# Kernel tuning notes

Measured on AMD Instinct MI355X. Metric: run time of the kernel, lower is better.

The kernel has to match this reference:

```python
import jax, jax.numpy as jnp
import numpy as np

# Balanced binary-tree tensorized circuit (CP sum-product layers), cirkit-style.
B, D, C, K, NCLS = 256, 256, 1, 256, 10
LEVELS = 8  # log2(D); each level halves the number of regions


def setup_inputs() -> dict:
    key = jax.random.key(0)
    ks = jax.random.split(key, LEVELS + 3)
    inp = {"x": jax.random.normal(ks[0], (B, D, C), dtype=jnp.float32)}
    # Input layer params: per-variable linear map C -> K units
    inp["W_in"] = jax.random.normal(ks[1], (D, C, K), dtype=jnp.float32)
    # CP layer params per tree level: (n_regions, arity=2, K_in, K_out)
    n = D
    for l in range(LEVELS):
        n //= 2
        inp[f"W_lvl{l}"] = jax.random.normal(ks[2 + l], (n, 2, K, K), dtype=jnp.float32)
    # Output mixing layer K -> num_classes
    inp["W_out"] = jax.random.normal(ks[2 + LEVELS], (K, NCLS), dtype=jnp.float32)
    return inp


def _circuit(x, W_in, W_lvls, W_out):
    # Input layers: gather scope (here: each var is its own scope) + per-var map.
    # (B, D, C) x (D, C, K) -> (B, D, K); tanh keeps units bounded in [-1, 1].
    h = jnp.tanh(jnp.einsum('bdc,dck->bdk', x, W_in))
    # Fused sum-product (CP) layers, one batched einsum per tree level instead of
    # a Python loop over individual small layers.
    for W in W_lvls:
        n = W.shape[0]
        hp = h.reshape(h.shape[0], n, 2, K)          # pair adjacent regions
        Wn = jax.nn.softmax(W, axis=2)               # reparam: convex sum over K_in
        proj = jnp.einsum('bnak,nakj->bnaj', hp, Wn) # per-child sum layer
        h = proj[:, :, 0, :] * proj[:, :, 1, :]      # Hadamard product layer
    root = h[:, 0, :]                                # (B, K)
    out = jnp.einsum('bk,kc->bc', root, jax.nn.softmax(W_out, axis=0))
    return out[:, None, :]                           # (B, num_out=1, num_cls)


def reference(x, W_in, W_lvl0, W_lvl1, W_lvl2, W_lvl3, W_lvl4, W_lvl5, W_lvl6, W_lvl7, W_out):
    W_lvls = [W_lvl0, W_lvl1, W_lvl2, W_lvl3, W_lvl4, W_lvl5, W_lvl6, W_lvl7]
    return _circuit(x, W_in, W_lvls, W_out)
```

## Files before the change

kernel.cpp:

```cpp
#include <hip/hip_runtime.h>

#define Bb 256
#define Kk 256
#define NCLS 10

typedef __attribute__((ext_vector_type(8))) short short8;
typedef __attribute__((ext_vector_type(4))) float f32x4;

__device__ __forceinline__ float bf2f(ushort u) {
    return __uint_as_float(((unsigned int)u) << 16);
}
__device__ __forceinline__ ushort f2bf(float f) {
    unsigned int u = __float_as_uint(f);
    u = (u + 0x7FFFu + ((u >> 16) & 1u)) >> 16;
    return (ushort)u;
}
__device__ __forceinline__ float tanh_fast(float v) {
    float t = __expf(2.f * v);
    return (t - 1.f) / (t + 1.f);
}

template<bool FIRST>
__global__ __launch_bounds__(256, 2)
void level_kernel(const float*  __restrict__ x,
                  const float*  __restrict__ Win,
                  const ushort* __restrict__ proj_prev,
                  const float*  __restrict__ W,
                  ushort*       __restrict__ proj_out,
                  int n)
{
    __shared__ __align__(16) ushort sA[256 * 40];
    __shared__ __align__(16) ushort sE[128 * 40];
    __shared__ float sRed[2][128];
    __shared__ float sRcp[128];

    const int tid = threadIdx.x;
    const int a   = blockIdx.x >> 1;
    const int jt  = blockIdx.x & 1;
    const int i   = blockIdx.y;
    const int d   = 2 * i + a;

    const int l   = tid & 63;
    const int l15 = l & 15;
    const int g   = l >> 4;
    const int w   = tid >> 6;
    const int wm  = w >> 1;
    const int wn  = w & 1;

    const int ej  = tid & 127;
    const int ekq = tid >> 7;

    f32x4 acc[8][4];
    #pragma unroll
    for (int mf = 0; mf < 8; ++mf)
        #pragma unroll
        for (int nf = 0; nf < 4; ++nf)
            acc[mf][nf] = (f32x4){0.f, 0.f, 0.f, 0.f};

    float csum = 0.f;

    const size_t wbase = ((size_t)(i * 2 + a)) * (size_t)(Kk * Kk);

    for (int k0 = 0; k0 < Kk; k0 += 32) {
        #pragma unroll
        for (int p = 0; p < 4; ++p) {
            const int unit = p * 256 + tid;
            const int m = unit >> 2;
            const int s = unit & 3;
            ushort pk[8];
            if (FIRST) {
                const float4 w0 = *(const float4*)&Win[(size_t)d * Kk + k0 + s * 8];
                const float4 w1 = *(const float4*)&Win[(size_t)d * Kk + k0 + s * 8 + 4];
                const float xv = x[(size_t)m * 256 + d];
                pk[0] = f2bf(tanh_fast(xv * w0.x));
                pk[1] = f2bf(tanh_fast(xv * w0.y));
                pk[2] = f2bf(tanh_fast(xv * w0.z));
                pk[3] = f2bf(tanh_fast(xv * w0.w));
                pk[4] = f2bf(tanh_fast(xv * w1.x));
                pk[5] = f2bf(tanh_fast(xv * w1.y));
                pk[6] = f2bf(tanh_fast(xv * w1.z));
                pk[7] = f2bf(tanh_fast(xv * w1.w));
            } else {
                const size_t base = (((size_t)m * (2 * n) + d) * 2) * 256 + k0 + s * 8;
                const short8 p0 = *(const short8*)&proj_prev[base];
                const short8 p1 = *(const short8*)&proj_prev[base + 256];
                #pragma unroll
                for (int e = 0; e < 8; ++e)
                    pk[e] = f2bf(bf2f((ushort)p0[e]) * bf2f((ushort)p1[e]));
            }
            short8 v;
            #pragma unroll
            for (int e = 0; e < 8; ++e) v[e] = (short)pk[e];
            *(short8*)&sA[m * 40 + s * 8] = v;
        }

        #pragma unroll
        for (int h2 = 0; h2 < 2; ++h2) {
            const int kk = ekq * 16 + h2 * 8;
            ushort pk[8];
            #pragma unroll
            for (int r = 0; r < 8; ++r) {
                const float wv = W[wbase + (size_t)(k0 + kk + r) * 256 + jt * 128 + ej];
                const float e = __expf(wv);
                csum += e;
                pk[r] = f2bf(e);
            }
            short8 v;
            #pragma unroll
            for (int e = 0; e < 8; ++e) v[e] = (short)pk[e];
            *(short8*)&sE[ej * 40 + kk] = v;
        }
        __syncthreads();

        short8 bfr[4];
        #pragma unroll
        for (int nf = 0; nf < 4; ++nf)
            bfr[nf] = *(const short8*)&sE[(wn * 64 + nf * 16 + l15) * 40 + g * 8];
        #pragma unroll
        for (int mf = 0; mf < 8; ++mf) {
            const short8 afr = *(const short8*)&sA[(wm * 128 + mf * 16 + l15) * 40 + g * 8];
            #pragma unroll
            for (int nf = 0; nf < 4; ++nf)
                acc[mf][nf] = __builtin_amdgcn_mfma_f32_16x16x32_bf16(
                    afr, bfr[nf], acc[mf][nf], 0, 0, 0);
        }
        __syncthreads();
    }

    sRed[ekq][ej] = csum;
    __syncthreads();
    if (tid < 128) sRcp[tid] = 1.f / (sRed[0][tid] + sRed[1][tid]);
    __syncthreads();

    float rj[4];
    #pragma unroll
    for (int nf = 0; nf < 4; ++nf) rj[nf] = sRcp[wn * 64 + nf * 16 + l15];

    #pragma unroll
    for (int mf = 0; mf < 8; ++mf)
        #pragma unroll
        for (int nf = 0; nf < 4; ++nf) {
            const int jloc = wn * 64 + nf * 16 + l15;
            #pragma unroll
            for (int r = 0; r < 4; ++r) {
                const int b = wm * 128 + mf * 16 + g * 4 + r;
                const size_t off = (((size_t)b * n + i) * 2 + a) * 256 + jt * 128 + jloc;
                proj_out[off] = f2bf(acc[mf][nf][r] * rj[nf]);
            }
        }
}

__global__ __launch_bounds__(256)
void out_kernel(const ushort* __restrict__ proj7,
                const float*  __restrict__ Wout,
                float*        __restrict__ out)
{
    __shared__ float sR[16][260];
    __shared__ float sE[256][12];
    __shared__ float sDen[16];

    const int tid = threadIdx.x;
    if (tid < 16) sDen[tid] = 0.f;
    __syncthreads();

    float e[NCLS];
    #pragma unroll
    for (int c = 0; c < NCLS; ++c) {
        e[c] = __expf(Wout[(size_t)tid * NCLS + c]);
        sE[tid][c] = e[c];
    }
    #pragma unroll
    for (int c = 0; c < NCLS; ++c) {
        float v = e[c];
        for (int off = 32; off > 0; off >>= 1) v += __shfl_down(v, off);
        if ((tid & 63) == 0) atomicAdd(&sDen[c], v);
    }

    const int b0 = blockIdx.x * 16;
    #pragma unroll
    for (int v = 0; v < 4; ++v) {
        const int u = v * 256 + tid;
        const int row = u >> 6;
        const int c4 = (u & 63) * 4;
        const size_t base = (size_t)(b0 + row) * 512 + c4;
        const ushort4 p0 = *(const ushort4*)&proj7[base];
        const ushort4 p1 = *(const ushort4*)&proj7[base + 256];
        sR[row][c4 + 0] = bf2f(p0.x) * bf2f(p1.x);
        sR[row][c4 + 1] = bf2f(p0.y) * bf2f(p1.y);
        sR[row][c4 + 2] = bf2f(p0.z) * bf2f(p1.z);
        sR[row][c4 + 3] = bf2f(p0.w) * bf2f(p1.w);
    }
    __syncthreads();

    const int ty = tid >> 4, tx = tid & 15;
    if (tx < NCLS) {
        float s = 0.f;
        for (int k = 0; k < Kk; ++k) s += sR[ty][k] * sE[k][tx];
        out[(size_t)(b0 + ty) * NCLS + tx] = s / sDen[tx];
    }
}

extern "C" void kernel_launch(void* const* d_in, const int* in_sizes, int n_in,
                              void* d_out, int out_size, void* d_ws, size_t ws_size,
                              hipStream_t stream)
{
    const float* x    = (const float*)d_in[0];
    const float* Win  = (const float*)d_in[1];
    const float* Wl[8];
    for (int lv = 0; lv < 8; ++lv) Wl[lv] = (const float*)d_in[2 + lv];
    const float* Wout = (const float*)d_in[10];
    float* out = (float*)d_out;

    ushort* P0 = (ushort*)d_ws;
    ushort* P1 = P0 + 16777216;

    level_kernel<true><<<dim3(4, 128), 256, 0, stream>>>(x, Win, nullptr, Wl[0], P0, 128);

    const ushort* cur = P0;
    for (int lv = 1; lv < 8; ++lv) {
        const int n = 128 >> lv;
        ushort* dst = (lv & 1) ? P1 : P0;
        level_kernel<false><<<dim3(4, n), 256, 0, stream>>>(nullptr, nullptr, cur, Wl[lv], dst, n);
        cur = dst;
    }

    out_kernel<<<dim3(16), 256, 0, stream>>>(cur, Wout, out);
}
```

Baseline: 333.0 us.

## Split batch tiles and use split-K with atomics for deep tree levels

```diff
diff --git a/kernel.cpp b/kernel.cpp
--- a/kernel.cpp
+++ b/kernel.cpp
@@ -20,25 +20,33 @@
     return (t - 1.f) / (t + 1.f);
 }
 
-template<bool FIRST>
-__global__ __launch_bounds__(256, 2)
+template<int MIN_, bool RAWOUT>
+__global__ __launch_bounds__(256, 3)
 void level_kernel(const float*  __restrict__ x,
                   const float*  __restrict__ Win,
-                  const ushort* __restrict__ proj_prev,
+                  const ushort* __restrict__ Pprev,
+                  const float*  __restrict__ Rprev,
+                  const float*  __restrict__ Cprev,
                   const float*  __restrict__ W,
-                  ushort*       __restrict__ proj_out,
-                  int n)
+                  ushort*       __restrict__ Pout,
+                  float*        __restrict__ Rout,
+                  float*        __restrict__ Cout,
+                  int n, int kchunk)
 {
-    __shared__ __align__(16) ushort sA[256 * 40];
+    __shared__ __align__(16) ushort sA[128 * 40];
     __shared__ __align__(16) ushort sE[128 * 40];
     __shared__ float sRed[2][128];
     __shared__ float sRcp[128];
 
     const int tid = threadIdx.x;
-    const int a   = blockIdx.x >> 1;
-    const int jt  = blockIdx.x & 1;
+    const int bh  = blockIdx.x & 1;
+    const int jt  = (blockIdx.x >> 1) & 1;
+    const int a   = blockIdx.x >> 2;
     const int i   = blockIdx.y;
     const int d   = 2 * i + a;
+    const int b0  = bh * 128;
+    const int j0  = jt * 128;
+    const int np  = 2 * n;
 
     const int l   = tid & 63;
     const int l15 = l & 15;
@@ -50,28 +58,29 @@
     const int ej  = tid & 127;
     const int ekq = tid >> 7;
 
-    f32x4 acc[8][4];
+    f32x4 acc[4][4];
     #pragma unroll
-    for (int mf = 0; mf < 8; ++mf)
+    for (int mf = 0; mf < 4; ++mf)
         #pragma unroll
         for (int nf = 0; nf < 4; ++nf)
             acc[mf][nf] = (f32x4){0.f, 0.f, 0.f, 0.f};
 
     float csum = 0.f;
-
     const size_t wbase = ((size_t)(i * 2 + a)) * (size_t)(Kk * Kk);
-
-    for (int k0 = 0; k0 < Kk; k0 += 32) {
-        #pragma unroll
-        for (int p = 0; p < 4; ++p) {
+    const int kb = blockIdx.z * kchunk;
+
+    for (int k0 = kb; k0 < kb + kchunk; k0 += 32) {
+        #pragma unroll
+        for (int p = 0; p < 2; ++p) {
             const int unit = p * 256 + tid;
             const int m = unit >> 2;
             const int s = unit & 3;
+            const int b = b0 + m;
             ushort pk[8];
-            if (FIRST) {
+            if (MIN_ == 0) {
                 const float4 w0 = *(const float4*)&Win[(size_t)d * Kk + k0 + s * 8];
                 const float4 w1 = *(const float4*)&Win[(size_t)d * Kk + k0 + s * 8 + 4];
-                const float xv = x[(size_t)m * 256 + d];
+                const float xv = x[(size_t)b * 256 + d];
                 pk[0] = f2bf(tanh_fast(xv * w0.x));
                 pk[1] = f2bf(tanh_fast(xv * w0.y));
                 pk[2] = f2bf(tanh_fast(xv * w0.z));
@@ -80,13 +89,31 @@
                 pk[5] = f2bf(tanh_fast(xv * w1.y));
                 pk[6] = f2bf(tanh_fast(xv * w1.z));
                 pk[7] = f2bf(tanh_fast(xv * w1.w));
-            } else {
-                const size_t base = (((size_t)m * (2 * n) + d) * 2) * 256 + k0 + s * 8;
-                const short8 p0 = *(const short8*)&proj_prev[base];
-                const short8 p1 = *(const short8*)&proj_prev[base + 256];
+            } else if (MIN_ == 1) {
+                const size_t base = (((size_t)b * np + d) * 2) * 256 + k0 + s * 8;
+                const short8 p0 = *(const short8*)&Pprev[base];
+                const short8 p1 = *(const short8*)&Pprev[base + 256];
                 #pragma unroll
                 for (int e = 0; e < 8; ++e)
                     pk[e] = f2bf(bf2f((ushort)p0[e]) * bf2f((ushort)p1[e]));
+            } else {
+                const size_t base = (((size_t)b * np + d) * 2) * 256 + k0 + s * 8;
+                const float4 p0a = *(const float4*)&Rprev[base];
+                const float4 p0b = *(const float4*)&Rprev[base + 4];
+                const float4 p1a = *(const float4*)&Rprev[base + 256];
+                const float4 p1b = *(const float4*)&Rprev[base + 260];
+                const size_t cb = (size_t)(d * 2) * 256 + k0 + s * 8;
+                const float4 c0a = *(const float4*)&Cprev[cb];
+                const float4 c0b = *(const float4*)&Cprev[cb + 4];
+                const float4 c1a = *(const float4*)&Cprev[cb + 256];
+                const float4 c1b = *(const float4*)&Cprev[cb + 260];
+                const float p0r[8] = {p0a.x,p0a.y,p0a.z,p0a.w,p0b.x,p0b.y,p0b.z,p0b.w};
+                const float p1r[8] = {p1a.x,p1a.y,p1a.z,p1a.w,p1b.x,p1b.y,p1b.z,p1b.w};
+                const float c0r[8] = {c0a.x,c0a.y,c0a.z,c0a.w,c0b.x,c0b.y,c0b.z,c0b.w};
+                const float c1r[8] = {c1a.x,c1a.y,c1a.z,c1a.w,c1b.x,c1b.y,c1b.z,c1b.w};
+                #pragma unroll
+                for (int e = 0; e < 8; ++e)
+                    pk[e] = f2bf((p0r[e] * p1r[e]) / (c0r[e] * c1r[e]));
             }
             short8 v;
             #pragma unroll
@@ -100,7 +127,7 @@
             ushort pk[8];
             #pragma unroll
             for (int r = 0; r < 8; ++r) {
-                const float wv = W[wbase + (size_t)(k0 + kk + r) * 256 + jt * 128 + ej];
+                const float wv = W[wbase + (size_t)(k0 + kk + r) * 256 + j0 + ej];
                 const float e = __expf(wv);
                 csum += e;
                 pk[r] = f2bf(e);
@@ -117,8 +144,8 @@
         for (int nf = 0; nf < 4; ++nf)
             bfr[nf] = *(const short8*)&sE[(wn * 64 + nf * 16 + l15) * 40 + g * 8];
         #pragma unroll
-        for (int mf = 0; mf < 8; ++mf) {
-            const short8 afr = *(const short8*)&sA[(wm * 128 + mf * 16 + l15) * 40 + g * 8];
+        for (int mf = 0; mf < 4; ++mf) {
+            const short8 afr = *(const short8*)&sA[(wm * 64 + mf * 16 + l15) * 40 + g * 8];
             #pragma unroll
             for (int nf = 0; nf < 4; ++nf)
                 acc[mf][nf] = __builtin_amdgcn_mfma_f32_16x16x32_bf16(
@@ -129,31 +156,60 @@
 
     sRed[ekq][ej] = csum;
     __syncthreads();
-    if (tid < 128) sRcp[tid] = 1.f / (sRed[0][tid] + sRed[1][tid]);
-    __syncthreads();
-
-    float rj[4];
-    #pragma unroll
-    for (int nf = 0; nf < 4; ++nf) rj[nf] = sRcp[wn * 64 + nf * 16 + l15];
-
-    #pragma unroll
-    for (int mf = 0; mf < 8; ++mf)
-        #pragma unroll
-        for (int nf = 0; nf < 4; ++nf) {
-            const int jloc = wn * 64 + nf * 16 + l15;
-            #pragma unroll
-            for (int r = 0; r < 4; ++r) {
-                const int b = wm * 128 + mf * 16 + g * 4 + r;
-                const size_t off = (((size_t)b * n + i) * 2 + a) * 256 + jt * 128 + jloc;
-                proj_out[off] = f2bf(acc[mf][nf][r] * rj[nf]);
+    if (!RAWOUT) {
+        if (tid < 128) sRcp[tid] = 1.f / (sRed[0][tid] + sRed[1][tid]);
+        __syncthreads();
+    } else {
+        if (tid < 128) {
+            const float cpart = sRed[0][tid] + sRed[1][tid];
+            atomicAdd(&Cout[(size_t)(i * 2 + a) * 256 + j0 + tid], cpart);
+        }
+    }
+
+    if (!RAWOUT) {
+        float rj[4];
+        #pragma unroll
+        for (int nf = 0; nf < 4; ++nf) rj[nf] = sRcp[wn * 64 + nf * 16 + l15];
+        #pragma unroll
+        for (int mf = 0; mf < 4; ++mf)
+            #pragma unroll
+            for (int nf = 0; nf < 4; ++nf) {
+                const int jl = wn * 64 + nf * 16 + l15;
+                #pragma unroll
+                for (int r = 0; r < 4; ++r) {
+                    const int b = b0 + wm * 64 + mf * 16 + g * 4 + r;
+                    const size_t off = (((size_t)b * n + i) * 2 + a) * 256 + j0 + jl;
+                    Pout[off] = f2bf(acc[mf][nf][r] * rj[nf]);
+                }
             }
-        }
+    } else {
+        #pragma unroll
+        for (int mf = 0; mf < 4; ++mf)
+            #pragma unroll
+            for (int nf = 0; nf < 4; ++nf) {
+                const int jl = wn * 64 + nf * 16 + l15;
+                #pragma unroll
+                for (int r = 0; r < 4; ++r) {
+                    const int b = b0 + wm * 64 + mf * 16 + g * 4 + r;
+                    const size_t off = (((size_t)b * n + i) * 2 + a) * 256 + j0 + jl;
+                    atomicAdd(&Rout[off], acc[mf][nf][r]);
+                }
+            }
+    }
+}
+
+__global__ void zero_kernel(float4* __restrict__ p, int n4)
+{
+    int idx = blockIdx.x * blockDim.x + threadIdx.x;
+    const int stride = gridDim.x * blockDim.x;
+    for (; idx < n4; idx += stride) p[idx] = (float4){0.f, 0.f, 0.f, 0.f};
 }
 
 __global__ __launch_bounds__(256)
-void out_kernel(const ushort* __restrict__ proj7,
-                const float*  __restrict__ Wout,
-                float*        __restrict__ out)
+void out_kernel(const float* __restrict__ R7,
+                const float* __restrict__ C7,
+                const float* __restrict__ Wout,
+                float*       __restrict__ out)
 {
     __shared__ float sR[16][260];
     __shared__ float sE[256][12];
@@ -183,12 +239,14 @@
         const int row = u >> 6;
         const int c4 = (u & 63) * 4;
         const size_t base = (size_t)(b0 + row) * 512 + c4;
-        const ushort4 p0 = *(const ushort4*)&proj7[base];
-        const ushort4 p1 = *(const ushort4*)&proj7[base + 256];
-        sR[row][c4 + 0] = bf2f(p0.x) * bf2f(p1.x);
-        sR[row][c4 + 1] = bf2f(p0.y) * bf2f(p1.y);
-        sR[row][c4 + 2] = bf2f(p0.z) * bf2f(p1.z);
-        sR[row][c4 + 3] = bf2f(p0.w) * bf2f(p1.w);
+        const float4 p0 = *(const float4*)&R7[base];
+        const float4 p1 = *(const float4*)&R7[base + 256];
+        const float4 c0 = *(const float4*)&C7[c4];
+        const float4 c1 = *(const float4*)&C7[256 + c4];
+        sR[row][c4 + 0] = (p0.x * p1.x) / (c0.x * c1.x);
+        sR[row][c4 + 1] = (p0.y * p1.y) / (c0.y * c1.y);
+        sR[row][c4 + 2] = (p0.z * p1.z) / (c0.z * c1.z);
+        sR[row][c4 + 3] = (p0.w * p1.w) / (c0.w * c1.w);
     }
     __syncthreads();
 
@@ -211,18 +269,40 @@
     const float* Wout = (const float*)d_in[10];
     float* out = (float*)d_out;
 
-    ushort* P0 = (ushort*)d_ws;
-    ushort* P1 = P0 + 16777216;
-
-    level_kernel<true><<<dim3(4, 128), 256, 0, stream>>>(x, Win, nullptr, Wl[0], P0, 128);
-
-    const ushort* cur = P0;
-    for (int lv = 1; lv < 8; ++lv) {
-        const int n = 128 >> lv;
-        ushort* dst = (lv & 1) ? P1 : P0;
-        level_kernel<false><<<dim3(4, n), 256, 0, stream>>>(nullptr, nullptr, cur, Wl[lv], dst, n);
-        cur = dst;
-    }
-
-    out_kernel<<<dim3(16), 256, 0, stream>>>(cur, Wout, out);
-}
+    char* wsb = (char*)d_ws;
+    const size_t MB = 1024 * 1024;
+    ushort* P0 = (ushort*)(wsb + 0);
+    ushort* P1 = (ushort*)(wsb + 32 * MB);
+    ushort* P2 = (ushort*)(wsb + 0);
+    ushort* P3 = (ushort*)(wsb + 8 * MB);
+    float* R4 = (float*)(wsb + 12 * MB);
+    float* C4 = (float*)(wsb + 16 * MB);
+    float* R5 = (float*)(wsb + 17 * MB);
+    float* C5 = (float*)(wsb + 19 * MB);
+    float* R6 = (float*)(wsb + 20 * MB);
+    float* C6 = (float*)(wsb + 21 * MB);
+    float* R7 = (float*)(wsb + 22 * MB);
+    float* C7 = (float*)(wsb + 23 * MB);
+
+    zero_kernel<<<1024, 256, 0, stream>>>((float4*)(wsb + 12 * MB),
+                                          (int)(12 * MB / 16));
+
+    level_kernel<0, false><<<dim3(8, 128, 1), 256, 0, stream>>>(
+        x, Win, nullptr, nullptr, nullptr, Wl[0], P0, nullptr, nullptr, 128, 256);
+    level_kernel<1, false><<<dim3(8, 64, 1), 256, 0, stream>>>(
+        nullptr, nullptr, P0, nullptr, nullptr, Wl[1], P1, nullptr, nullptr, 64, 256);
+    level_kernel<1, false><<<dim3(8, 32, 1), 256, 0, stream>>>(
+        nullptr, nullptr, P1, nullptr, nullptr, Wl[2], P2, nullptr, nullptr, 32, 256);
+    level_kernel<1, false><<<dim3(8, 16, 1), 256, 0, stream>>>(
+        nullptr, nullptr, P2, nullptr, nullptr, Wl[3], P3, nullptr, nullptr, 16, 256);
+    level_kernel<1, true><<<dim3(8, 8, 4), 256, 0, stream>>>(
+        nullptr, nullptr, P3, nullptr, nullptr, Wl[4], nullptr, R4, C4, 8, 64);
+    level_kernel<2, true><<<dim3(8, 4, 8), 256, 0, stream>>>(
+        nullptr, nullptr, nullptr, R4, C4, Wl[5], nullptr, R5, C5, 4, 32);
+    level_kernel<2, true><<<dim3(8, 2, 8), 256, 0, stream>>>(
+        nullptr, nullptr, nullptr, R5, C5, Wl[6], nullptr, R6, C6, 2, 32);
+    level_kernel<2, true><<<dim3(8, 1, 8), 256, 0, stream>>>(
+        nullptr, nullptr, nullptr, R6, C6, Wl[7], nullptr, R7, C7, 1, 32);
+
+    out_kernel<<<dim3(16), 256, 0, stream>>>(R7, C7, Wout, out);
+}
```

After: 398.7 us. 1.2x slower.

## Precompute softmax exp weights in separate kernels and fuse Hadamard into level GEMM epilogue

Applied to the files above, without the earlier changes.

```diff
diff --git a/kernel.cpp b/kernel.cpp
--- a/kernel.cpp
+++ b/kernel.cpp
@@ -1,6 +1,6 @@
 #include <hip/hip_runtime.h>
-
-#define Bb 256
+#include <stdint.h>
+
 #define Kk 256
 #define NCLS 10
 
@@ -19,26 +19,107 @@
     float t = __expf(2.f * v);
     return (t - 1.f) / (t + 1.f);
 }
-
-template<bool FIRST>
-__global__ __launch_bounds__(256, 2)
-void level_kernel(const float*  __restrict__ x,
-                  const float*  __restrict__ Win,
-                  const ushort* __restrict__ proj_prev,
-                  const float*  __restrict__ W,
-                  ushort*       __restrict__ proj_out,
-                  int n)
-{
-    __shared__ __align__(16) ushort sA[256 * 40];
-    __shared__ __align__(16) ushort sE[128 * 40];
-    __shared__ float sRed[2][128];
-    __shared__ float sRcp[128];
-
+__device__ __forceinline__ void gll16(const void* g, void* s) {
+    __builtin_amdgcn_global_load_lds(
+        (const __attribute__((address_space(1))) void*)g,
+        (__attribute__((address_space(3))) void*)s, 16, 0, 0);
+}
+
+__device__ void exp_tile(const float* __restrict__ Wb, ushort* __restrict__ Eb,
+                         float* __restrict__ rcp_row, const int j0)
+{
+    __shared__ float sT[64][68];
+    __shared__ float sC[4][64];
     const int tid = threadIdx.x;
-    const int a   = blockIdx.x >> 1;
-    const int jt  = blockIdx.x & 1;
+    const int lj = tid & 63;
+    const int kq = tid >> 6;
+    const int jj = (tid & 15) * 4;
+    const int kk = tid >> 4;
+    float csum = 0.f;
+
+    for (int kb = 0; kb < 4; ++kb) {
+        #pragma unroll
+        for (int p = 0; p < 4; ++p) {
+            const int k = kb * 64 + p * 16 + kk;
+            *(float4*)&sT[p * 16 + kk][jj] = *(const float4*)&Wb[(size_t)k * 256 + j0 + jj];
+        }
+        __syncthreads();
+        ushort pk[16];
+        #pragma unroll
+        for (int t = 0; t < 16; ++t) {
+            const float e = __expf(sT[kq * 16 + t][lj]);
+            csum += e;
+            pk[t] = f2bf(e);
+        }
+        short8 v0, v1;
+        #pragma unroll
+        for (int e2 = 0; e2 < 8; ++e2) { v0[e2] = (short)pk[e2]; v1[e2] = (short)pk[8 + e2]; }
+        ushort* dst = Eb + (size_t)(j0 + lj) * 256 + kb * 64 + kq * 16;
+        *(short8*)dst = v0;
+        *(short8*)(dst + 8) = v1;
+        __syncthreads();
+    }
+    sC[kq][lj] = csum;
+    __syncthreads();
+    if (tid < 64)
+        rcp_row[j0 + tid] = 1.f / (sC[0][tid] + sC[1][tid] + sC[2][tid] + sC[3][tid]);
+}
+
+__global__ __launch_bounds__(256)
+void exp0_kernel(const float* __restrict__ W, ushort* __restrict__ E,
+                 float* __restrict__ Rcp)
+{
+    const int ia = blockIdx.y;
+    const int j0 = blockIdx.x * 64;
+    exp_tile(W + (size_t)ia * 65536, E + ((size_t)ia << 16),
+             Rcp + (size_t)ia * 256, j0);
+}
+
+__global__ __launch_bounds__(256)
+void exp_rest_kernel(const float* __restrict__ W1, const float* __restrict__ W2,
+                     const float* __restrict__ W3, const float* __restrict__ W4,
+                     const float* __restrict__ W5, const float* __restrict__ W6,
+                     const float* __restrict__ W7,
+                     ushort* __restrict__ Ebase, float* __restrict__ RcpBase)
+{
+    int rem = blockIdx.x;
+    int lvl = 1, n2 = 128;
+    while (rem >= n2 * 4 && lvl < 7) { rem -= n2 * 4; n2 >>= 1; ++lvl; }
+    const int jt = rem & 3;
+    const int ia = rem >> 2;
+    const float* W;
+    switch (lvl) {
+        case 1: W = W1; break; case 2: W = W2; break; case 3: W = W3; break;
+        case 4: W = W4; break; case 5: W = W5; break; case 6: W = W6; break;
+        default: W = W7; break;
+    }
+    size_t eoff = 0; int rrow = 256;
+    for (int m = 1; m < lvl; ++m) { eoff += ((size_t)(256 >> m)) << 16; rrow += (256 >> m); }
+    exp_tile(W + (size_t)ia * 65536,
+             Ebase + eoff + ((size_t)ia << 16),
+             RcpBase + (size_t)(rrow + ia) * 256, jt * 64);
+}
+
+template<bool TANH>
+__global__ __launch_bounds__(256, 3)
+void level_kernel(const float* __restrict__ x,
+                  const float* __restrict__ Win,
+                  const ushort* __restrict__ H,
+                  const ushort* __restrict__ E,
+                  const float* __restrict__ Rcp,
+                  ushort* __restrict__ Hout,
+                  const int n)
+{
+    __shared__ __align__(16) char sA[2][2][128 * 64];
+    __shared__ __align__(16) char sE[2][2][64 * 64];
+
+    const int tid = threadIdx.x;
+    const int bh  = blockIdx.x & 1;
+    const int jt  = blockIdx.x >> 1;
     const int i   = blockIdx.y;
-    const int d   = 2 * i + a;
+    const int b0  = bh * 128;
+    const int j0  = jt * 64;
+    const int np  = 2 * n;
 
     const int l   = tid & 63;
     const int l15 = l & 15;
@@ -47,127 +128,138 @@
     const int wm  = w >> 1;
     const int wn  = w & 1;
 
-    const int ej  = tid & 127;
-    const int ekq = tid >> 7;
-
-    f32x4 acc[8][4];
-    #pragma unroll
-    for (int mf = 0; mf < 8; ++mf)
-        #pragma unroll
-        for (int nf = 0; nf < 4; ++nf)
-            acc[mf][nf] = (f32x4){0.f, 0.f, 0.f, 0.f};
-
-    float csum = 0.f;
-
-    const size_t wbase = ((size_t)(i * 2 + a)) * (size_t)(Kk * Kk);
-
-    for (int k0 = 0; k0 < Kk; k0 += 32) {
-        #pragma unroll
-        for (int p = 0; p < 4; ++p) {
-            const int unit = p * 256 + tid;
-            const int m = unit >> 2;
-            const int s = unit & 3;
-            ushort pk[8];
-            if (FIRST) {
-                const float4 w0 = *(const float4*)&Win[(size_t)d * Kk + k0 + s * 8];
-                const float4 w1 = *(const float4*)&Win[(size_t)d * Kk + k0 + s * 8 + 4];
-                const float xv = x[(size_t)m * 256 + d];
-                pk[0] = f2bf(tanh_fast(xv * w0.x));
-                pk[1] = f2bf(tanh_fast(xv * w0.y));
-                pk[2] = f2bf(tanh_fast(xv * w0.z));
-                pk[3] = f2bf(tanh_fast(xv * w0.w));
-                pk[4] = f2bf(tanh_fast(xv * w1.x));
-                pk[5] = f2bf(tanh_fast(xv * w1.y));
-                pk[6] = f2bf(tanh_fast(xv * w1.z));
-                pk[7] = f2bf(tanh_fast(xv * w1.w));
-            } else {
-                const size_t base = (((size_t)m * (2 * n) + d) * 2) * 256 + k0 + s * 8;
-                const short8 p0 = *(const short8*)&proj_prev[base];
-                const short8 p1 = *(const short8*)&proj_prev[base + 256];
+    f32x4 acc[2][4][2];
+    #pragma unroll
+    for (int a2 = 0; a2 < 2; ++a2)
+        #pragma unroll
+        for (int mf = 0; mf < 4; ++mf)
+            #pragma unroll
+            for (int nf = 0; nf < 2; ++nf)
+                acc[a2][mf][nf] = (f32x4){0.f, 0.f, 0.f, 0.f};
+
+    float xv = 0.f;
+    const int ta   = tid >> 7;
+    const int trow = tid & 127;
+    if (TANH) xv = x[(size_t)(b0 + trow) * 256 + (2 * i + ta)];
+
+    auto stage = [&](int buf, int k0) {
+        if (TANH) {
+            const float* wrow = &Win[(size_t)(2 * i + ta) * 256 + k0];
+            char* base = &sA[ta][buf][trow * 64];
+            const int sr = (trow >> 1) & 3;
+            #pragma unroll
+            for (int c = 0; c < 4; ++c) {
+                const float4 w0 = *(const float4*)&wrow[c * 8];
+                const float4 w1 = *(const float4*)&wrow[c * 8 + 4];
+                short8 v;
+                v[0] = (short)f2bf(tanh_fast(xv * w0.x));
+                v[1] = (short)f2bf(tanh_fast(xv * w0.y));
+                v[2] = (short)f2bf(tanh_fast(xv * w0.z));
+                v[3] = (short)f2bf(tanh_fast(xv * w0.w));
+                v[4] = (short)f2bf(tanh_fast(xv * w1.x));
+                v[5] = (short)f2bf(tanh_fast(xv * w1.y));
+                v[6] = (short)f2bf(tanh_fast(xv * w1.z));
+                v[7] = (short)f2bf(tanh_fast(xv * w1.w));
+                *(short8*)(base + (((c ^ sr)) << 4)) = v;
+            }
+        } else {
+            #pragma unroll
+            for (int u0 = 0; u0 < 4; ++u0) {
+                const int u   = w * 4 + u0;
+                const int ua  = u >> 3;
+                const int r16 = (u & 7) << 4;
+                const int row = r16 + (l >> 2);
+                const int c   = l & 3;
+                const ushort* src = H
+                    + ((size_t)(b0 + row) * np + (2 * i + ua)) * 256
+                    + k0 + ((c ^ ((row >> 1) & 3)) << 3);
+                gll16(src, &sA[ua][buf][r16 * 64]);
+            }
+        }
+        #pragma unroll
+        for (int v0 = 0; v0 < 2; ++v0) {
+            const int v    = w * 2 + v0;
+            const int ea   = v >> 2;
+            const int jr16 = (v & 3) << 4;
+            const int jr   = jr16 + (l >> 2);
+            const int c    = l & 3;
+            const ushort* src = E + ((size_t)(2 * i + ea) << 16)
+                + (size_t)(j0 + jr) * 256
+                + k0 + ((c ^ ((jr >> 1) & 3)) << 3);
+            gll16(src, &sE[ea][buf][jr16 * 64]);
+        }
+    };
+
+    stage(0, 0);
+    __syncthreads();
+
+    for (int t = 0; t < 8; ++t) {
+        const int buf = t & 1;
+        if (t < 7) stage(buf ^ 1, (t + 1) * 32);
+
+        short8 afr[2][4];
+        short8 bfr[2][2];
+        #pragma unroll
+        for (int a2 = 0; a2 < 2; ++a2) {
+            #pragma unroll
+            for (int nf = 0; nf < 2; ++nf) {
+                const int jr = wn * 32 + nf * 16 + l15;
+                bfr[a2][nf] = *(const short8*)&sE[a2][buf][jr * 64 + ((g ^ ((jr >> 1) & 3)) << 4)];
+            }
+            #pragma unroll
+            for (int mf = 0; mf < 4; ++mf) {
+                const int row = wm * 64 + mf * 16 + l15;
+                afr[a2][mf] = *(const short8*)&sA[a2][buf][row * 64 + ((g ^ ((row >> 1) & 3)) << 4)];
+            }
+        }
+        #pragma unroll
+        for (int a2 = 0; a2 < 2; ++a2)
+            #pragma unroll
+            for (int mf = 0; mf < 4; ++mf)
                 #pragma unroll
-                for (int e = 0; e < 8; ++e)
-                    pk[e] = f2bf(bf2f((ushort)p0[e]) * bf2f((ushort)p1[e]));
-            }
-            short8 v;
-            #pragma unroll
-            for (int e = 0; e < 8; ++e) v[e] = (short)pk[e];
-            *(short8*)&sA[m * 40 + s * 8] = v;
-        }
-
-        #pragma unroll
-        for (int h2 = 0; h2 < 2; ++h2) {
-            const int kk = ekq * 16 + h2 * 8;
-            ushort pk[8];
-            #pragma unroll
-            for (int r = 0; r < 8; ++r) {
-                const float wv = W[wbase + (size_t)(k0 + kk + r) * 256 + jt * 128 + ej];
-                const float e = __expf(wv);
-                csum += e;
-                pk[r] = f2bf(e);
-            }
-            short8 v;
-            #pragma unroll
-            for (int e = 0; e < 8; ++e) v[e] = (short)pk[e];
-            *(short8*)&sE[ej * 40 + kk] = v;
-        }
+                for (int nf = 0; nf < 2; ++nf)
+                    acc[a2][mf][nf] = __builtin_amdgcn_mfma_f32_16x16x32_bf16(
+                        afr[a2][mf], bfr[a2][nf], acc[a2][mf][nf], 0, 0, 0);
         __syncthreads();
-
-        short8 bfr[4];
-        #pragma unroll
-        for (int nf = 0; nf < 4; ++nf)
-            bfr[nf] = *(const short8*)&sE[(wn * 64 + nf * 16 + l15) * 40 + g * 8];
-        #pragma unroll
-        for (int mf = 0; mf < 8; ++mf) {
-            const short8 afr = *(const short8*)&sA[(wm * 128 + mf * 16 + l15) * 40 + g * 8];
-            #pragma unroll
-            for (int nf = 0; nf < 4; ++nf)
-                acc[mf][nf] = __builtin_amdgcn_mfma_f32_16x16x32_bf16(
-                    afr, bfr[nf], acc[mf][nf], 0, 0, 0);
-        }
-        __syncthreads();
-    }
-
-    sRed[ekq][ej] = csum;
-    __syncthreads();
-    if (tid < 128) sRcp[tid] = 1.f / (sRed[0][tid] + sRed[1][tid]);
-    __syncthreads();
-
-    float rj[4];
-    #pragma unroll
-    for (int nf = 0; nf < 4; ++nf) rj[nf] = sRcp[wn * 64 + nf * 16 + l15];
-
-    #pragma unroll
-    for (int mf = 0; mf < 8; ++mf)
-        #pragma unroll
-        for (int nf = 0; nf < 4; ++nf) {
-            const int jloc = wn * 64 + nf * 16 + l15;
+    }
+
+    float rc[2][2];
+    #pragma unroll
+    for (int a2 = 0; a2 < 2; ++a2)
+        #pragma unroll
+        for (int nf = 0; nf < 2; ++nf)
+            rc[a2][nf] = Rcp[(size_t)(2 * i + a2) * 256 + j0 + wn * 32 + nf * 16 + l15];
+
+    #pragma unroll
+    for (int mf = 0; mf < 4; ++mf)
+        #pragma unroll
+        for (int nf = 0; nf < 2; ++nf) {
+            const int j = j0 + wn * 32 + nf * 16 + l15;
             #pragma unroll
             for (int r = 0; r < 4; ++r) {
-                const int b = wm * 128 + mf * 16 + g * 4 + r;
-                const size_t off = (((size_t)b * n + i) * 2 + a) * 256 + jt * 128 + jloc;
-                proj_out[off] = f2bf(acc[mf][nf][r] * rj[nf]);
+                const int b = b0 + wm * 64 + mf * 16 + g * 4 + r;
+                const float v0 = acc[0][mf][nf][r] * rc[0][nf];
+                const float v1 = acc[1][mf][nf][r] * rc[1][nf];
+                Hout[((size_t)b * n + i) * 256 + j] = f2bf(v0 * v1);
             }
         }
 }
 
 __global__ __launch_bounds__(256)
-void out_kernel(const ushort* __restrict__ proj7,
-                const float*  __restrict__ Wout,
-                float*        __restrict__ out)
+void out_kernel(const ushort* __restrict__ root, const float* __restrict__ Wout,
+                float* __restrict__ out)
 {
     __shared__ float sR[16][260];
-    __shared__ float sE[256][12];
+    __shared__ float sE2[256][12];
     __shared__ float sDen[16];
-
     const int tid = threadIdx.x;
     if (tid < 16) sDen[tid] = 0.f;
     __syncthreads();
-
     float e[NCLS];
     #pragma unroll
     for (int c = 0; c < NCLS; ++c) {
         e[c] = __expf(Wout[(size_t)tid * NCLS + c]);
-        sE[tid][c] = e[c];
+        sE2[tid][c] = e[c];
     }
     #pragma unroll
     for (int c = 0; c < NCLS; ++c) {
@@ -175,27 +267,23 @@
         for (int off = 32; off > 0; off >>= 1) v += __shfl_down(v, off);
         if ((tid & 63) == 0) atomicAdd(&sDen[c], v);
     }
-
     const int b0 = blockIdx.x * 16;
     #pragma unroll
     for (int v = 0; v < 4; ++v) {
         const int u = v * 256 + tid;
         const int row = u >> 6;
         const int c4 = (u & 63) * 4;
-        const size_t base = (size_t)(b0 + row) * 512 + c4;
-        const ushort4 p0 = *(const ushort4*)&proj7[base];
-        const ushort4 p1 = *(const ushort4*)&proj7[base + 256];
-        sR[row][c4 + 0] = bf2f(p0.x) * bf2f(p1.x);
-        sR[row][c4 + 1] = bf2f(p0.y) * bf2f(p1.y);
-        sR[row][c4 + 2] = bf2f(p0.z) * bf2f(p1.z);
-        sR[row][c4 + 3] = bf2f(p0.w) * bf2f(p1.w);
+        const ushort4 p = *(const ushort4*)&root[(size_t)(b0 + row) * 256 + c4];
+        sR[row][c4 + 0] = bf2f(p.x);
+        sR[row][c4 + 1] = bf2f(p.y);
+        sR[row][c4 + 2] = bf2f(p.z);
+        sR[row][c4 + 3] = bf2f(p.w);
     }
     __syncthreads();
-
     const int ty = tid >> 4, tx = tid & 15;
     if (tx < NCLS) {
         float s = 0.f;
-        for (int k = 0; k < Kk; ++k) s += sR[ty][k] * sE[k][tx];
+        for (int k = 0; k < Kk; ++k) s += sR[ty][k] * sE2[k][tx];
         out[(size_t)(b0 + ty) * NCLS + tx] = s / sDen[tx];
     }
 }
@@ -211,18 +299,28 @@
     const float* Wout = (const float*)d_in[10];
     float* out = (float*)d_out;
 
-    ushort* P0 = (ushort*)d_ws;
-    ushort* P1 = P0 + 16777216;
-
-    level_kernel<true><<<dim3(4, 128), 256, 0, stream>>>(x, Win, nullptr, Wl[0], P0, 128);
-
-    const ushort* cur = P0;
+    char* wsb = (char*)d_ws;
+    ushort* R1 = (ushort*)wsb;
+    ushort* R2 = (ushort*)(wsb + 33554432);
+    ushort* R3 = (ushort*)(wsb + 50331648);
+    float*  RC = (float*)(wsb + 58720256);
+
+    exp0_kernel<<<dim3(4, 256), 256, 0, stream>>>(Wl[0], R1, RC);
+    level_kernel<true><<<dim3(8, 128), 256, 0, stream>>>(x, Win, nullptr, R1, RC, R2, 128);
+    exp_rest_kernel<<<dim3(1016), 256, 0, stream>>>(Wl[1], Wl[2], Wl[3], Wl[4],
+                                                    Wl[5], Wl[6], Wl[7], R1, RC);
+    size_t eoff = 0;
+    size_t rrow = 256;
+    const ushort* hin = R2;
+    ushort* hout = nullptr;
     for (int lv = 1; lv < 8; ++lv) {
         const int n = 128 >> lv;
-        ushort* dst = (lv & 1) ? P1 : P0;
-        level_kernel<false><<<dim3(4, n), 256, 0, stream>>>(nullptr, nullptr, cur, Wl[lv], dst, n);
-        cur = dst;
-    }
-
-    out_kernel<<<dim3(16), 256, 0, stream>>>(cur, Wout, out);
-}
+        hout = (lv & 1) ? R3 : R2;
+        level_kernel<false><<<dim3(8, n), 256, 0, stream>>>(
+            nullptr, nullptr, hin, R1 + eoff, RC + rrow * 256, hout, n);
+        hin = hout;
+        eoff += ((size_t)(2 * n)) << 16;
+        rrow += 2 * n;
+    }
+    out_kernel<<<dim3(16), 256, 0, stream>>>(hin, Wout, out);
+}
```

New measurement: 313.8 us. 1.06x faster.
